# Kernel optimization log

Hardware: AMD Instinct MI355X
Metric: run time of the kernel (lower is better)

The kernel has to match this reference:

```python
import jax, jax.numpy as jnp
import numpy as np

B, N, F_DIM = 64, 4096, 64
K_SLOTS, D, N_ITERS = 8, 64, 3
EPS = 1e-8
LN_EPS = 1e-5  # torch LayerNorm default


def layernorm(x, g, b):
    mu = jnp.mean(x, axis=-1, keepdims=True)
    var = jnp.mean(jnp.square(x - mu), axis=-1, keepdims=True)
    return (x - mu) * jax.lax.rsqrt(var + LN_EPS) * g + b


def gru_cell(x, h, w_ih, w_hh, b_ih, b_hh):
    # torch.nn.GRUCell semantics; weights are [3D, D] with gate order r, z, n
    gi = x @ w_ih.T + b_ih
    gh = h @ w_hh.T + b_hh
    i_r, i_z, i_n = jnp.split(gi, 3, axis=-1)
    h_r, h_z, h_n = jnp.split(gh, 3, axis=-1)
    r = jax.nn.sigmoid(i_r + h_r)
    z = jax.nn.sigmoid(i_z + h_z)
    n = jnp.tanh(i_n + r * h_n)
    return (1.0 - z) * n + z * h


def setup_inputs() -> dict:
    key = jax.random.key(0)
    ks = jax.random.split(key, 16)
    f32 = jnp.float32
    s = 0.05  # small init scale for weights
    return {
        "inputs": jax.random.normal(ks[0], (B, N, F_DIM), f32),
        "slots_noise": jax.random.normal(ks[1], (B, K_SLOTS, D), f32),
        "slots_mu": jax.random.normal(ks[2], (1, 1, D), f32) * s,
        "slots_log_sigma": jax.random.normal(ks[3], (1, 1, D), f32) * s,
        "Wq": jax.random.normal(ks[4], (D, D), f32) * s,
        "Wk": jax.random.normal(ks[5], (D, F_DIM), f32) * s,
        "Wv": jax.random.normal(ks[6], (D, F_DIM), f32) * s,
        "gru_w_ih": jax.random.normal(ks[7], (3 * D, D), f32) * s,
        "gru_w_hh": jax.random.normal(ks[8], (3 * D, D), f32) * s,
        "gru_b_ih": jnp.zeros((3 * D,), f32),
        "gru_b_hh": jnp.zeros((3 * D,), f32),
        "mlp_w1": jax.random.normal(ks[9], (2 * D, D), f32) * s,
        "mlp_b1": jnp.zeros((2 * D,), f32),
        "mlp_w2": jax.random.normal(ks[10], (D, 2 * D), f32) * s,
        "mlp_b2": jnp.zeros((D,), f32),
        "ln_in_g": jnp.ones((F_DIM,), f32), "ln_in_b": jnp.zeros((F_DIM,), f32),
        "ln_slots_g": jnp.ones((D,), f32), "ln_slots_b": jnp.zeros((D,), f32),
        "ln_mlp_g": jnp.ones((D,), f32), "ln_mlp_b": jnp.zeros((D,), f32),
    }


def reference(inputs, slots_noise, slots_mu, slots_log_sigma, Wq, Wk, Wv,
              gru_w_ih, gru_w_hh, gru_b_ih, gru_b_hh,
              mlp_w1, mlp_b1, mlp_w2, mlp_b2,
              ln_in_g, ln_in_b, ln_slots_g, ln_slots_b, ln_mlp_g, ln_mlp_b):
    x = layernorm(inputs, ln_in_g, ln_in_b)          # [B, N, F]
    k = jnp.einsum('bnf,df->bnd', x, Wk)             # [B, N, D]
    v = jnp.einsum('bnf,df->bnd', x, Wv)             # [B, N, D]

    slots = slots_mu + jnp.exp(slots_log_sigma) * slots_noise  # [B, K, D]
    scale = D ** -0.5

    for _ in range(N_ITERS):
        slots_prev = slots
        s_n = layernorm(slots, ln_slots_g, ln_slots_b)
        q = jnp.einsum('bkd,ed->bke', s_n, Wq)                  # [B, K, D]
        attn_logits = jnp.einsum('bnd,bkd->bnk', k, q) * scale  # [B, N, K]
        attn = jax.nn.softmax(attn_logits, axis=-1) + EPS       # softmax over slots
        attn = attn / jnp.sum(attn, axis=1, keepdims=True)      # renormalize over N
        updates = jnp.einsum('bnk,bnd->bkd', attn, v)           # [B, K, D]
        slots = gru_cell(updates.reshape(-1, D), slots_prev.reshape(-1, D),
                         gru_w_ih, gru_w_hh, gru_b_ih, gru_b_hh).reshape(B, K_SLOTS, D)
        h = layernorm(slots, ln_mlp_g, ln_mlp_b)
        h = jax.nn.relu(h @ mlp_w1.T + mlp_b1) @ mlp_w2.T + mlp_b2
        slots = slots + h
    return slots
```

## Files before the change

### kernel.cpp

```cpp
#include <hip/hip_runtime.h>
#include <math.h>

#define NN 4096
#define LN_EPS 1e-5f
#define EPS 1e-8f

typedef unsigned short ushortT;
typedef unsigned int uintT;
typedef __attribute__((ext_vector_type(8))) short short8;
typedef __attribute__((ext_vector_type(4))) float f32x4;
typedef __attribute__((ext_vector_type(4))) unsigned short us4;

#define OFF_KT    0L
#define OFF_V     16777216L
#define OFF_QT    33554432L
#define OFF_ACC   33587200L
#define OFF_COL   33619968L
#define OFF_SLOTS 33620480L
#define OFF_WIHT  33653248L
#define OFF_WHHT  33665536L
#define OFF_W1T   33677824L
#define OFF_W2T   33686016L
#define OFF_WQT   33694208L
#define OFF_WKV   33698304L

__device__ __forceinline__ float wredsum(float v) {
#pragma unroll
  for (int off = 32; off > 0; off >>= 1) v += __shfl_xor(v, off);
  return v;
}

__device__ __forceinline__ ushortT f2bf(float f) {
  uintT b = __float_as_uint(f);
  b += 0x7fff + ((b >> 16) & 1);
  return (ushortT)(b >> 16);
}

__global__ __launch_bounds__(256) void k_prep(
    const float* __restrict__ w_ih, const float* __restrict__ w_hh,
    const float* __restrict__ w1, const float* __restrict__ w2,
    const float* __restrict__ Wq,
    const float* __restrict__ Wk, const float* __restrict__ Wv,
    float* __restrict__ wihT, float* __restrict__ whhT,
    float* __restrict__ w1T, float* __restrict__ w2T, float* __restrict__ wqT,
    ushortT* __restrict__ wpack)
{
  int idx = blockIdx.x * 256 + threadIdx.x;
  if (idx < 12288) {
    int j = idx >> 6, f = idx & 63;
    wihT[f * 192 + j] = w_ih[idx];
  } else if (idx < 24576) {
    int i = idx - 12288; int j = i >> 6, f = i & 63;
    whhT[f * 192 + j] = w_hh[i];
  } else if (idx < 32768) {
    int i = idx - 24576; int j = i >> 6, f = i & 63;
    w1T[f * 128 + j] = w1[i];
  } else if (idx < 40960) {
    int i = idx - 32768; int d = i >> 7, j = i & 127;
    w2T[j * 64 + d] = w2[i];
  } else if (idx < 45056) {
    int i = idx - 40960; int e = i >> 6, d = i & 63;
    wqT[d * 64 + e] = Wq[i];
  } else if (idx < 53248) {
    int i = idx - 45056;
    int j = i & 7, l = (i >> 3) & 63, t2 = i >> 9;
    int ct = t2 >> 1, kb = t2 & 1;
    int kf = kb * 32 + ((l >> 4) << 3) + j;
    int col = (ct << 4) | (l & 15);
    float val = (col < 64) ? Wk[col * 64 + kf] : Wv[(col - 64) * 64 + kf];
    wpack[i] = f2bf(val);
  }
}

__global__ __launch_bounds__(256) void k_ln_project(
    const float* __restrict__ inp, const ushortT* __restrict__ wpack,
    const float* __restrict__ g, const float* __restrict__ bbv,
    ushortT* __restrict__ ktF, ushortT* __restrict__ vF)
{
  __shared__ __align__(16) ushortT xnF[4096];
  __shared__ __align__(16) ushortT kS[4096];
  const int tid = threadIdx.x;
  const int lane = tid & 63;
  const int wave = tid >> 6;
  const int l15 = lane & 15, q = lane >> 4;
  const int tile = blockIdx.x;
  const int b = tile >> 6;
  const int c = tile & 63;
  const int n0 = c << 6;
  const float* rowbase = inp + (((long)b * NN + n0) << 6);
  const float4 g4 = *(const float4*)&g[l15 << 2];
  const float4 b4 = *(const float4*)&bbv[l15 << 2];

#pragma unroll
  for (int i = 0; i < 4; ++i) {
    const int row = (wave << 4) + (i << 2) + q;
    float4 x = *(const float4*)&rowbase[(row << 6) + (l15 << 2)];
    float s = x.x + x.y + x.z + x.w;
    s += __shfl_xor(s, 1); s += __shfl_xor(s, 2);
    s += __shfl_xor(s, 4); s += __shfl_xor(s, 8);
    const float mu = s * (1.f / 64.f);
    float4 dx = {x.x - mu, x.y - mu, x.z - mu, x.w - mu};
    float ss = dx.x * dx.x + dx.y * dx.y + dx.z * dx.z + dx.w * dx.w;
    ss += __shfl_xor(ss, 1); ss += __shfl_xor(ss, 2);
    ss += __shfl_xor(ss, 4); ss += __shfl_xor(ss, 8);
    const float rs = rsqrtf(ss * (1.f / 64.f) + LN_EPS);
    us4 p = {f2bf(dx.x * rs * g4.x + b4.x), f2bf(dx.y * rs * g4.y + b4.y),
             f2bf(dx.z * rs * g4.z + b4.z), f2bf(dx.w * rs * g4.w + b4.w)};
    *(us4*)&xnF[((((wave << 1) + (l15 >> 3)) << 6) + (((l15 & 7) >> 1) << 4)
                 + (row & 15)) * 8 + ((l15 & 1) << 2)] = p;
  }

  short8 bfrag[2][2];
#pragma unroll
  for (int nt = 0; nt < 2; ++nt)
#pragma unroll
    for (int kb = 0; kb < 2; ++kb)
      bfrag[nt][kb] = *(const short8*)&wpack[((((2 * wave + nt) << 1) | kb) * 64 + lane) << 3];

  __syncthreads();

  f32x4 acc[4][2];
#pragma unroll
  for (int mt = 0; mt < 4; ++mt)
#pragma unroll
    for (int nt = 0; nt < 2; ++nt) acc[mt][nt] = (f32x4){0.f, 0.f, 0.f, 0.f};

#pragma unroll
  for (int mt = 0; mt < 4; ++mt) {
    short8 a0 = *(const short8*)&xnF[((mt * 2 + 0) * 64 + lane) << 3];
    short8 a1 = *(const short8*)&xnF[((mt * 2 + 1) * 64 + lane) << 3];
#pragma unroll
    for (int nt = 0; nt < 2; ++nt) {
      acc[mt][nt] = __builtin_amdgcn_mfma_f32_16x16x32_bf16(a0, bfrag[nt][0], acc[mt][nt], 0, 0, 0);
      acc[mt][nt] = __builtin_amdgcn_mfma_f32_16x16x32_bf16(a1, bfrag[nt][1], acc[mt][nt], 0, 0, 0);
    }
  }

  if (wave < 2) {
#pragma unroll
    for (int mt = 0; mt < 4; ++mt)
#pragma unroll
      for (int nt = 0; nt < 2; ++nt) {
        const int base = (((mt * 2 + wave) << 6) + ((2 * nt + (l15 >> 3)) << 4) + (q << 2));
#pragma unroll
        for (int r = 0; r < 4; ++r)
          kS[((base + r) << 3) + (l15 & 7)] = f2bf(acc[mt][nt][r]);
      }
  } else {
    ushortT* vbase = vF + ((long)(b * 64 + c) << 12);
#pragma unroll
    for (int mt = 0; mt < 4; ++mt)
#pragma unroll
      for (int nt = 0; nt < 2; ++nt) {
        const int ntg = 2 * (wave - 2) + nt;
        us4 p = {f2bf(acc[mt][nt][0]), f2bf(acc[mt][nt][1]),
                 f2bf(acc[mt][nt][2]), f2bf(acc[mt][nt][3])};
        *(us4*)&vbase[(((((ntg << 1) + (mt >> 1)) << 6)
                        + (((mt & 1) * 2 + (q >> 1)) << 4) + l15) << 3)
                      + ((q & 1) << 2)] = p;
      }
  }
  __syncthreads();

  ushortT* kdst = ktF + ((long)(b * 64 + c) << 12);
  short8 v0 = *(const short8*)&kS[tid << 4];
  short8 v1 = *(const short8*)&kS[(tid << 4) + 8];
  *(short8*)&kdst[tid << 4] = v0;
  *(short8*)&kdst[(tid << 4) + 8] = v1;
}

__global__ __launch_bounds__(256) void k_init(
    const float* __restrict__ noise, const float* __restrict__ smu,
    const float* __restrict__ slsig, const float* __restrict__ wqT,
    const float* __restrict__ g_sl, const float* __restrict__ b_sl,
    float* __restrict__ slots, ushortT* __restrict__ qF,
    float* __restrict__ acc, float* __restrict__ colsum)
{
  __shared__ float S[4][64];
  const int tid = threadIdx.x, lane = tid & 63, wave = tid >> 6;
  const int row = blockIdx.x * 4 + wave;
  const int b = row >> 3, ks = row & 7;

  float s0 = fmaf(expf(slsig[lane]), noise[row * 64 + lane], smu[lane]);
  slots[row * 64 + lane] = s0;
  acc[row * 64 + lane] = 0.f;
  if (lane == 0) colsum[row] = 0.f;

  float mu = wredsum(s0) * (1.f / 64.f);
  float dx = s0 - mu;
  float var = wredsum(dx * dx) * (1.f / 64.f);
  float sn = dx * rsqrtf(var + LN_EPS) * g_sl[lane] + b_sl[lane];
  S[wave][lane] = sn;
  __syncthreads();
  float qe = 0.f;
#pragma unroll 16
  for (int d = 0; d < 64; ++d) qe = fmaf(S[wave][d], wqT[d * 64 + lane], qe);
  const int kb = lane >> 5, lrow = (lane & 31) >> 3, j = lane & 7;
  qF[((((b * 2 + kb) << 6) + (lrow << 4) + ks) << 3) + j] = f2bf(qe * 0.125f);
  qF[((((b * 2 + kb) << 6) + (lrow << 4) + 8 + ks) << 3) + j] = 0;
}

__global__ __launch_bounds__(256) void k_attn(
    const ushortT* __restrict__ ktF, const ushortT* __restrict__ vF,
    const ushortT* __restrict__ qF,
    float* __restrict__ acc, float* __restrict__ colsum)
{
  __shared__ __align__(16) ushortT attnF[4][1024];
  __shared__ float accLds[4][8][64];
  __shared__ float colLds[4][8];
  const int tid = threadIdx.x;
  const int lane = tid & 63;
  const int wave = tid >> 6;
  const int l15 = lane & 15, q = lane >> 4;
  const int b = blockIdx.x >> 4;
  const int chunk = ((blockIdx.x & 15) << 2) | wave;

  const ushortT* kbF = ktF + ((long)(b * 64 + chunk) << 12);
  const ushortT* vbF = vF + ((long)(b * 64 + chunk) << 12);

  short8 kA[4][2];
#pragma unroll
  for (int mt = 0; mt < 4; ++mt)
#pragma unroll
    for (int kb = 0; kb < 2; ++kb)
      kA[mt][kb] = *(const short8*)&kbF[((mt * 2 + kb) * 64 + lane) << 3];
  short8 qB[2];
#pragma unroll
  for (int kb = 0; kb < 2; ++kb)
    qB[kb] = *(const short8*)&qF[(((b * 2 + kb) << 6) + lane) << 3];

  f32x4 accL[4];
#pragma unroll
  for (int mt = 0; mt < 4; ++mt) {
    accL[mt] = (f32x4){0.f, 0.f, 0.f, 0.f};
    accL[mt] = __builtin_amdgcn_mfma_f32_16x16x32_bf16(kA[mt][0], qB[0], accL[mt], 0, 0, 0);
    accL[mt] = __builtin_amdgcn_mfma_f32_16x16x32_bf16(kA[mt][1], qB[1], accL[mt], 0, 0, 0);
  }

  short8 vB[4][2];
#pragma unroll
  for (int nt = 0; nt < 4; ++nt)
#pragma unroll
    for (int ks = 0; ks < 2; ++ks)
      vB[nt][ks] = *(const short8*)&vbF[((nt * 2 + ks) * 64 + lane) << 3];

  float csum = 0.f;
#pragma unroll
  for (int mt = 0; mt < 4; ++mt) {
    float av[4];
#pragma unroll
    for (int r = 0; r < 4; ++r) {
      float lv = accL[mt][r];
      float mx = lv;
      mx = fmaxf(mx, __shfl_xor(mx, 1));
      mx = fmaxf(mx, __shfl_xor(mx, 2));
      mx = fmaxf(mx, __shfl_xor(mx, 4));
      float ev = __expf(lv - mx);
      float sv = ev;
      sv += __shfl_xor(sv, 1); sv += __shfl_xor(sv, 2); sv += __shfl_xor(sv, 4);
      float a = ev * (1.f / sv) + EPS;
      av[r] = a;
      csum += a;
    }
    us4 p = {f2bf(av[0]), f2bf(av[1]), f2bf(av[2]), f2bf(av[3])};
    *(us4*)&attnF[wave][((((mt >> 1) << 6) + (((mt & 1) * 2 + (q >> 1)) << 4)
                          + l15) << 3) + ((q & 1) << 2)] = p;
  }
  csum += __shfl_xor(csum, 16);
  csum += __shfl_xor(csum, 32);

  short8 pA0 = *(const short8*)&attnF[wave][(0 * 64 + lane) << 3];
  short8 pA1 = *(const short8*)&attnF[wave][(1 * 64 + lane) << 3];

  f32x4 accP[4];
#pragma unroll
  for (int nt = 0; nt < 4; ++nt) {
    accP[nt] = (f32x4){0.f, 0.f, 0.f, 0.f};
    accP[nt] = __builtin_amdgcn_mfma_f32_16x16x32_bf16(pA0, vB[nt][0], accP[nt], 0, 0, 0);
    accP[nt] = __builtin_amdgcn_mfma_f32_16x16x32_bf16(pA1, vB[nt][1], accP[nt], 0, 0, 0);
  }

  if (q < 2) {
#pragma unroll
    for (int nt = 0; nt < 4; ++nt)
#pragma unroll
      for (int r = 0; r < 4; ++r)
        accLds[wave][q * 4 + r][nt * 16 + l15] = accP[nt][r];
  }
  if (q == 0 && l15 < 8) colLds[wave][l15] = csum;
  __syncthreads();

#pragma unroll
  for (int r = 0; r < 2; ++r) {
    const int o = tid + r * 256;
    const int kk = o >> 6, d = o & 63;
    float s = accLds[0][kk][d] + accLds[1][kk][d] + accLds[2][kk][d] + accLds[3][kk][d];
    atomicAdd(&acc[(b * 8 + kk) * 64 + d], s);
  }
  if (tid < 8) {
    float s = colLds[0][tid] + colLds[1][tid] + colLds[2][tid] + colLds[3][tid];
    atomicAdd(&colsum[b * 8 + tid], s);
  }
}

__global__ __launch_bounds__(256) void k_update(
    float* __restrict__ acc, float* __restrict__ colsum,
    float* __restrict__ slots,
    const float* __restrict__ wihT, const float* __restrict__ whhT,
    const float* __restrict__ w1T, const float* __restrict__ w2T,
    const float* __restrict__ wqT,
    const float* __restrict__ b_ih, const float* __restrict__ b_hh,
    const float* __restrict__ mb1, const float* __restrict__ mb2,
    const float* __restrict__ g_ml, const float* __restrict__ b_ml,
    const float* __restrict__ g_sl, const float* __restrict__ b_sl,
    ushortT* __restrict__ qF, float* __restrict__ dout)
{
  __shared__ float S[4][256];
  const int tid = threadIdx.x, lane = tid & 63, wave = tid >> 6;
  const int row = blockIdx.x * 4 + wave;
  const int b = row >> 3, ks = row & 7;

  const float csum = colsum[row];
  const float u = acc[row * 64 + lane] / csum;
  const float h = slots[row * 64 + lane];
  acc[row * 64 + lane] = 0.f;
  if (lane == 0) colsum[row] = 0.f;

  float* Su = &S[wave][0];
  float* Sh = &S[wave][64];
  Su[lane] = u; Sh[lane] = h;
  __syncthreads();

  float gir = b_ih[lane], giz = b_ih[64 + lane], gin = b_ih[128 + lane];
  float ghr = b_hh[lane], ghz = b_hh[64 + lane], ghn = b_hh[128 + lane];
#pragma unroll 4
  for (int f = 0; f < 64; ++f) {
    const float uf = Su[f], hf = Sh[f];
    gir = fmaf(uf, wihT[f * 192 + lane], gir);
    giz = fmaf(uf, wihT[f * 192 + 64 + lane], giz);
    gin = fmaf(uf, wihT[f * 192 + 128 + lane], gin);
    ghr = fmaf(hf, whhT[f * 192 + lane], ghr);
    ghz = fmaf(hf, whhT[f * 192 + 64 + lane], ghz);
    ghn = fmaf(hf, whhT[f * 192 + 128 + lane], ghn);
  }
  const float r = 1.f / (1.f + expf(-(gir + ghr)));
  const float z = 1.f / (1.f + expf(-(giz + ghz)));
  const float nn = tanhf(fmaf(r, ghn, gin));
  const float hnew = (1.f - z) * nn + z * h;

  float mu = wredsum(hnew) * (1.f / 64.f);
  float dx = hnew - mu;
  float var = wredsum(dx * dx) * (1.f / 64.f);
  const float ln = dx * rsqrtf(var + LN_EPS) * g_ml[lane] + b_ml[lane];
  float* Sln = &S[wave][128];
  Sln[lane] = ln;
  __syncthreads();

  float h1a = mb1[lane], h1b = mb1[64 + lane];
#pragma unroll 4
  for (int f = 0; f < 64; ++f) {
    const float lf = Sln[f];
    h1a = fmaf(lf, w1T[f * 128 + lane], h1a);
    h1b = fmaf(lf, w1T[f * 128 + 64 + lane], h1b);
  }
  h1a = fmaxf(h1a, 0.f); h1b = fmaxf(h1b, 0.f);
  __syncthreads();
  float* Shid = &S[wave][0];
  Shid[lane] = h1a; Shid[64 + lane] = h1b;
  __syncthreads();

  float o = mb2[lane];
#pragma unroll 4
  for (int j = 0; j < 128; ++j) o = fmaf(Shid[j], w2T[j * 64 + lane], o);
  const float snew = hnew + o;
  slots[row * 64 + lane] = snew;
  if (dout) dout[row * 64 + lane] = snew;

  float mu2 = wredsum(snew) * (1.f / 64.f);
  float dx2 = snew - mu2;
  float v2 = wredsum(dx2 * dx2) * (1.f / 64.f);
  const float sq = dx2 * rsqrtf(v2 + LN_EPS) * g_sl[lane] + b_sl[lane];
  __syncthreads();
  float* Ssq = &S[wave][128];
  Ssq[lane] = sq;
  __syncthreads();
  float qe = 0.f;
#pragma unroll 16
  for (int d = 0; d < 64; ++d) qe = fmaf(Ssq[d], wqT[d * 64 + lane], qe);
  const int kb = lane >> 5, lrow = (lane & 31) >> 3, j = lane & 7;
  qF[((((b * 2 + kb) << 6) + (lrow << 4) + ks) << 3) + j] = f2bf(qe * 0.125f);
}

extern "C" void kernel_launch(void* const* d_in, const int* in_sizes, int n_in,
                              void* d_out, int out_size, void* d_ws, size_t ws_size,
                              hipStream_t stream) {
  const float* inp   = (const float*)d_in[0];
  const float* noise = (const float*)d_in[1];
  const float* smu   = (const float*)d_in[2];
  const float* slsig = (const float*)d_in[3];
  const float* Wq    = (const float*)d_in[4];
  const float* Wk    = (const float*)d_in[5];
  const float* Wv    = (const float*)d_in[6];
  const float* w_ih  = (const float*)d_in[7];
  const float* w_hh  = (const float*)d_in[8];
  const float* b_ih  = (const float*)d_in[9];
  const float* b_hh  = (const float*)d_in[10];
  const float* w1    = (const float*)d_in[11];
  const float* b1    = (const float*)d_in[12];
  const float* w2    = (const float*)d_in[13];
  const float* b2    = (const float*)d_in[14];
  const float* g_in  = (const float*)d_in[15];
  const float* bi_in = (const float*)d_in[16];
  const float* g_sl  = (const float*)d_in[17];
  const float* bi_sl = (const float*)d_in[18];
  const float* g_ml  = (const float*)d_in[19];
  const float* bi_ml = (const float*)d_in[20];

  float* ws      = (float*)d_ws;
  ushortT* ktF   = (ushortT*)(ws + OFF_KT);
  ushortT* vF    = (ushortT*)(ws + OFF_V);
  ushortT* qF    = (ushortT*)(ws + OFF_QT);
  float* ac      = ws + OFF_ACC;
  float* cs      = ws + OFF_COL;
  float* sl      = ws + OFF_SLOTS;
  float* wihT    = ws + OFF_WIHT;
  float* whhT    = ws + OFF_WHHT;
  float* w1T     = ws + OFF_W1T;
  float* w2T     = ws + OFF_W2T;
  float* wqT     = ws + OFF_WQT;
  ushortT* wpk   = (ushortT*)(ws + OFF_WKV);

  k_prep<<<208, 256, 0, stream>>>(w_ih, w_hh, w1, w2, Wq, Wk, Wv,
                                  wihT, whhT, w1T, w2T, wqT, wpk);
  k_ln_project<<<4096, 256, 0, stream>>>(inp, wpk, g_in, bi_in, ktF, vF);
  k_init<<<128, 256, 0, stream>>>(noise, smu, slsig, wqT, g_sl, bi_sl, sl, qF, ac, cs);
  for (int it = 0; it < 3; ++it) {
    k_attn<<<1024, 256, 0, stream>>>(ktF, vF, qF, ac, cs);
    k_update<<<128, 256, 0, stream>>>(ac, cs, sl, wihT, whhT, w1T, w2T, wqT,
                                      b_ih, b_hh, b1, b2, g_ml, bi_ml, g_sl, bi_sl,
                                      qF, it == 2 ? (float*)d_out : nullptr);
  }
}
```

Baseline: 243.3 us.

## Fuse slot update into attention via last-block counter and merge init into LN kernel

Removes the separate k_update launch by having the last of the 16 attention blocks per batch, detected with an atomic counter, perform the GRU, MLP and next-query computation, two slots per wave. It also folds the slot initialisation into the LN/projection kernel as extra blocks, which cuts two launches per iteration structure down to one. The cost is a tail of serial update work on a single block per batch, plus threadfence and atomic overhead. The counter must be reset correctly for the next iteration.

```diff
diff --git a/kernel.cpp b/kernel.cpp
--- a/kernel.cpp
+++ b/kernel.cpp
@@ -23,6 +23,7 @@
 #define OFF_W2T   33686016L
 #define OFF_WQT   33694208L
 #define OFF_WKV   33698304L
+#define OFF_CNT   33702400L
 
 __device__ __forceinline__ float wredsum(float v) {
 #pragma unroll
@@ -43,7 +44,7 @@
     const float* __restrict__ Wk, const float* __restrict__ Wv,
     float* __restrict__ wihT, float* __restrict__ whhT,
     float* __restrict__ w1T, float* __restrict__ w2T, float* __restrict__ wqT,
-    ushortT* __restrict__ wpack)
+    ushortT* __restrict__ wpack, uintT* __restrict__ cnt)
 {
   int idx = blockIdx.x * 256 + threadIdx.x;
   if (idx < 12288) {
@@ -69,19 +70,53 @@
     int col = (ct << 4) | (l & 15);
     float val = (col < 64) ? Wk[col * 64 + kf] : Wv[(col - 64) * 64 + kf];
     wpack[i] = f2bf(val);
-  }
-}
-
-__global__ __launch_bounds__(256) void k_ln_project(
+  } else if (idx < 53312) {
+    cnt[idx - 53248] = 0u;
+  }
+}
+
+__global__ __launch_bounds__(256) void k_ln_init(
     const float* __restrict__ inp, const ushortT* __restrict__ wpack,
     const float* __restrict__ g, const float* __restrict__ bbv,
-    ushortT* __restrict__ ktF, ushortT* __restrict__ vF)
+    ushortT* __restrict__ ktF, ushortT* __restrict__ vF,
+    const float* __restrict__ noise, const float* __restrict__ smu,
+    const float* __restrict__ slsig, const float* __restrict__ wqT,
+    const float* __restrict__ g_sl, const float* __restrict__ b_sl,
+    float* __restrict__ slots, ushortT* __restrict__ qF,
+    float* __restrict__ acc, float* __restrict__ colsum)
 {
   __shared__ __align__(16) ushortT xnF[4096];
   __shared__ __align__(16) ushortT kS[4096];
   const int tid = threadIdx.x;
   const int lane = tid & 63;
   const int wave = tid >> 6;
+
+  if (blockIdx.x >= 4096) {
+    const int bi = blockIdx.x - 4096;
+    const int row = bi * 4 + wave;
+    const int b = row >> 3, ks = row & 7;
+    float* S2 = (float*)&xnF[0];
+
+    float s0 = fmaf(expf(slsig[lane]), noise[row * 64 + lane], smu[lane]);
+    slots[row * 64 + lane] = s0;
+    acc[row * 64 + lane] = 0.f;
+    if (lane == 0) colsum[row] = 0.f;
+
+    float mu = wredsum(s0) * (1.f / 64.f);
+    float dx = s0 - mu;
+    float var = wredsum(dx * dx) * (1.f / 64.f);
+    float sn = dx * rsqrtf(var + LN_EPS) * g_sl[lane] + b_sl[lane];
+    S2[(wave << 6) + lane] = sn;
+    __syncthreads();
+    float qe = 0.f;
+#pragma unroll 16
+    for (int d = 0; d < 64; ++d) qe = fmaf(S2[(wave << 6) + d], wqT[d * 64 + lane], qe);
+    const int kb = lane >> 5, lrow = (lane & 31) >> 3, j = lane & 7;
+    qF[((((b * 2 + kb) << 6) + (lrow << 4) + ks) << 3) + j] = f2bf(qe * 0.125f);
+    qF[((((b * 2 + kb) << 6) + (lrow << 4) + 8 + ks) << 3) + j] = 0;
+    return;
+  }
+
   const int l15 = lane & 15, q = lane >> 4;
   const int tile = blockIdx.x;
   const int b = tile >> 6;
@@ -119,11 +154,11 @@
 
   __syncthreads();
 
-  f32x4 acc[4][2];
+  f32x4 acc4[4][2];
 #pragma unroll
   for (int mt = 0; mt < 4; ++mt)
 #pragma unroll
-    for (int nt = 0; nt < 2; ++nt) acc[mt][nt] = (f32x4){0.f, 0.f, 0.f, 0.f};
+    for (int nt = 0; nt < 2; ++nt) acc4[mt][nt] = (f32x4){0.f, 0.f, 0.f, 0.f};
 
 #pragma unroll
   for (int mt = 0; mt < 4; ++mt) {
@@ -131,8 +166,8 @@
     short8 a1 = *(const short8*)&xnF[((mt * 2 + 1) * 64 + lane) << 3];
 #pragma unroll
     for (int nt = 0; nt < 2; ++nt) {
-      acc[mt][nt] = __builtin_amdgcn_mfma_f32_16x16x32_bf16(a0, bfrag[nt][0], acc[mt][nt], 0, 0, 0);
-      acc[mt][nt] = __builtin_amdgcn_mfma_f32_16x16x32_bf16(a1, bfrag[nt][1], acc[mt][nt], 0, 0, 0);
+      acc4[mt][nt] = __builtin_amdgcn_mfma_f32_16x16x32_bf16(a0, bfrag[nt][0], acc4[mt][nt], 0, 0, 0);
+      acc4[mt][nt] = __builtin_amdgcn_mfma_f32_16x16x32_bf16(a1, bfrag[nt][1], acc4[mt][nt], 0, 0, 0);
     }
   }
 
@@ -144,7 +179,7 @@
         const int base = (((mt * 2 + wave) << 6) + ((2 * nt + (l15 >> 3)) << 4) + (q << 2));
 #pragma unroll
         for (int r = 0; r < 4; ++r)
-          kS[((base + r) << 3) + (l15 & 7)] = f2bf(acc[mt][nt][r]);
+          kS[((base + r) << 3) + (l15 & 7)] = f2bf(acc4[mt][nt][r]);
       }
   } else {
     ushortT* vbase = vF + ((long)(b * 64 + c) << 12);
@@ -153,8 +188,8 @@
 #pragma unroll
       for (int nt = 0; nt < 2; ++nt) {
         const int ntg = 2 * (wave - 2) + nt;
-        us4 p = {f2bf(acc[mt][nt][0]), f2bf(acc[mt][nt][1]),
-                 f2bf(acc[mt][nt][2]), f2bf(acc[mt][nt][3])};
+        us4 p = {f2bf(acc4[mt][nt][0]), f2bf(acc4[mt][nt][1]),
+                 f2bf(acc4[mt][nt][2]), f2bf(acc4[mt][nt][3])};
         *(us4*)&vbase[(((((ntg << 1) + (mt >> 1)) << 6)
                         + (((mt & 1) * 2 + (q >> 1)) << 4) + l15) << 3)
                       + ((q & 1) << 2)] = p;
@@ -169,45 +204,24 @@
   *(short8*)&kdst[(tid << 4) + 8] = v1;
 }
 
-__global__ __launch_bounds__(256) void k_init(
-    const float* __restrict__ noise, const float* __restrict__ smu,
-    const float* __restrict__ slsig, const float* __restrict__ wqT,
-    const float* __restrict__ g_sl, const float* __restrict__ b_sl,
-    float* __restrict__ slots, ushortT* __restrict__ qF,
-    float* __restrict__ acc, float* __restrict__ colsum)
-{
-  __shared__ float S[4][64];
-  const int tid = threadIdx.x, lane = tid & 63, wave = tid >> 6;
-  const int row = blockIdx.x * 4 + wave;
-  const int b = row >> 3, ks = row & 7;
-
-  float s0 = fmaf(expf(slsig[lane]), noise[row * 64 + lane], smu[lane]);
-  slots[row * 64 + lane] = s0;
-  acc[row * 64 + lane] = 0.f;
-  if (lane == 0) colsum[row] = 0.f;
-
-  float mu = wredsum(s0) * (1.f / 64.f);
-  float dx = s0 - mu;
-  float var = wredsum(dx * dx) * (1.f / 64.f);
-  float sn = dx * rsqrtf(var + LN_EPS) * g_sl[lane] + b_sl[lane];
-  S[wave][lane] = sn;
-  __syncthreads();
-  float qe = 0.f;
-#pragma unroll 16
-  for (int d = 0; d < 64; ++d) qe = fmaf(S[wave][d], wqT[d * 64 + lane], qe);
-  const int kb = lane >> 5, lrow = (lane & 31) >> 3, j = lane & 7;
-  qF[((((b * 2 + kb) << 6) + (lrow << 4) + ks) << 3) + j] = f2bf(qe * 0.125f);
-  qF[((((b * 2 + kb) << 6) + (lrow << 4) + 8 + ks) << 3) + j] = 0;
-}
-
 __global__ __launch_bounds__(256) void k_attn(
     const ushortT* __restrict__ ktF, const ushortT* __restrict__ vF,
-    const ushortT* __restrict__ qF,
-    float* __restrict__ acc, float* __restrict__ colsum)
+    ushortT* __restrict__ qF,
+    float* __restrict__ acc, float* __restrict__ colsum,
+    uintT* __restrict__ cnt, float* __restrict__ slots,
+    const float* __restrict__ wihT, const float* __restrict__ whhT,
+    const float* __restrict__ w1T, const float* __restrict__ w2T,
+    const float* __restrict__ wqT,
+    const float* __restrict__ b_ih, const float* __restrict__ b_hh,
+    const float* __restrict__ mb1, const float* __restrict__ mb2,
+    const float* __restrict__ g_ml, const float* __restrict__ b_ml,
+    const float* __restrict__ g_sl, const float* __restrict__ b_sl,
+    float* __restrict__ dout)
 {
   __shared__ __align__(16) ushortT attnF[4][1024];
   __shared__ float accLds[4][8][64];
   __shared__ float colLds[4][8];
+  __shared__ int lastFlag;
   const int tid = threadIdx.x;
   const int lane = tid & 63;
   const int wave = tid >> 6;
@@ -301,94 +315,121 @@
     float s = colLds[0][tid] + colLds[1][tid] + colLds[2][tid] + colLds[3][tid];
     atomicAdd(&colsum[b * 8 + tid], s);
   }
-}
-
-__global__ __launch_bounds__(256) void k_update(
-    float* __restrict__ acc, float* __restrict__ colsum,
-    float* __restrict__ slots,
-    const float* __restrict__ wihT, const float* __restrict__ whhT,
-    const float* __restrict__ w1T, const float* __restrict__ w2T,
-    const float* __restrict__ wqT,
-    const float* __restrict__ b_ih, const float* __restrict__ b_hh,
-    const float* __restrict__ mb1, const float* __restrict__ mb2,
-    const float* __restrict__ g_ml, const float* __restrict__ b_ml,
-    const float* __restrict__ g_sl, const float* __restrict__ b_sl,
-    ushortT* __restrict__ qF, float* __restrict__ dout)
-{
-  __shared__ float S[4][256];
-  const int tid = threadIdx.x, lane = tid & 63, wave = tid >> 6;
-  const int row = blockIdx.x * 4 + wave;
-  const int b = row >> 3, ks = row & 7;
-
-  const float csum = colsum[row];
-  const float u = acc[row * 64 + lane] / csum;
-  const float h = slots[row * 64 + lane];
-  acc[row * 64 + lane] = 0.f;
-  if (lane == 0) colsum[row] = 0.f;
-
-  float* Su = &S[wave][0];
-  float* Sh = &S[wave][64];
-  Su[lane] = u; Sh[lane] = h;
+
+  __threadfence();
   __syncthreads();
-
-  float gir = b_ih[lane], giz = b_ih[64 + lane], gin = b_ih[128 + lane];
-  float ghr = b_hh[lane], ghz = b_hh[64 + lane], ghn = b_hh[128 + lane];
+  if (tid == 0) lastFlag = (atomicAdd(&cnt[b], 1u) == 15u);
+  __syncthreads();
+  if (!lastFlag) return;
+
+  const int ks0 = wave, ks1 = wave + 4;
+  const int row0 = b * 8 + ks0, row1 = b * 8 + ks1;
+
+  float csv0 = 0.f, csv1 = 0.f;
+  if (lane == 0) {
+    csv0 = atomicAdd(&colsum[row0], 0.f);
+    csv1 = atomicAdd(&colsum[row1], 0.f);
+  }
+  csv0 = __shfl(csv0, 0); csv1 = __shfl(csv1, 0);
+  const float u0 = atomicAdd(&acc[row0 * 64 + lane], 0.f) / csv0;
+  const float u1 = atomicAdd(&acc[row1 * 64 + lane], 0.f) / csv1;
+  const float h0 = slots[row0 * 64 + lane];
+  const float h1 = slots[row1 * 64 + lane];
+
+  float* S = (float*)&attnF[wave][0];
+  S[lane] = u0; S[64 + lane] = u1; S[128 + lane] = h0; S[192 + lane] = h1;
+
+  float gir0 = b_ih[lane], giz0 = b_ih[64 + lane], gin0 = b_ih[128 + lane];
+  float ghr0 = b_hh[lane], ghz0 = b_hh[64 + lane], ghn0 = b_hh[128 + lane];
+  float gir1 = gir0, giz1 = giz0, gin1 = gin0;
+  float ghr1 = ghr0, ghz1 = ghz0, ghn1 = ghn0;
 #pragma unroll 4
   for (int f = 0; f < 64; ++f) {
-    const float uf = Su[f], hf = Sh[f];
-    gir = fmaf(uf, wihT[f * 192 + lane], gir);
-    giz = fmaf(uf, wihT[f * 192 + 64 + lane], giz);
-    gin = fmaf(uf, wihT[f * 192 + 128 + lane], gin);
-    ghr = fmaf(hf, whhT[f * 192 + lane], ghr);
-    ghz = fmaf(hf, whhT[f * 192 + 64 + lane], ghz);
-    ghn = fmaf(hf, whhT[f * 192 + 128 + lane], ghn);
-  }
-  const float r = 1.f / (1.f + expf(-(gir + ghr)));
-  const float z = 1.f / (1.f + expf(-(giz + ghz)));
-  const float nn = tanhf(fmaf(r, ghn, gin));
-  const float hnew = (1.f - z) * nn + z * h;
-
-  float mu = wredsum(hnew) * (1.f / 64.f);
-  float dx = hnew - mu;
-  float var = wredsum(dx * dx) * (1.f / 64.f);
-  const float ln = dx * rsqrtf(var + LN_EPS) * g_ml[lane] + b_ml[lane];
-  float* Sln = &S[wave][128];
-  Sln[lane] = ln;
-  __syncthreads();
-
-  float h1a = mb1[lane], h1b = mb1[64 + lane];
+    const float wr = wihT[f * 192 + lane], wz = wihT[f * 192 + 64 + lane],
+                wn = wihT[f * 192 + 128 + lane];
+    const float vr = whhT[f * 192 + lane], vz = whhT[f * 192 + 64 + lane],
+                vn = whhT[f * 192 + 128 + lane];
+    const float a0 = S[f], a1 = S[64 + f], c0 = S[128 + f], c1 = S[192 + f];
+    gir0 = fmaf(a0, wr, gir0); gir1 = fmaf(a1, wr, gir1);
+    giz0 = fmaf(a0, wz, giz0); giz1 = fmaf(a1, wz, giz1);
+    gin0 = fmaf(a0, wn, gin0); gin1 = fmaf(a1, wn, gin1);
+    ghr0 = fmaf(c0, vr, ghr0); ghr1 = fmaf(c1, vr, ghr1);
+    ghz0 = fmaf(c0, vz, ghz0); ghz1 = fmaf(c1, vz, ghz1);
+    ghn0 = fmaf(c0, vn, ghn0); ghn1 = fmaf(c1, vn, ghn1);
+  }
+  const float r0 = 1.f / (1.f + expf(-(gir0 + ghr0)));
+  const float z0 = 1.f / (1.f + expf(-(giz0 + ghz0)));
+  const float n0 = tanhf(fmaf(r0, ghn0, gin0));
+  const float hn0 = (1.f - z0) * n0 + z0 * h0;
+  const float r1 = 1.f / (1.f + expf(-(gir1 + ghr1)));
+  const float z1 = 1.f / (1.f + expf(-(giz1 + ghz1)));
+  const float n1 = tanhf(fmaf(r1, ghn1, gin1));
+  const float hn1 = (1.f - z1) * n1 + z1 * h1;
+
+  float mu0 = wredsum(hn0) * (1.f / 64.f);
+  float dx0 = hn0 - mu0;
+  float va0 = wredsum(dx0 * dx0) * (1.f / 64.f);
+  const float ln0 = dx0 * rsqrtf(va0 + LN_EPS) * g_ml[lane] + b_ml[lane];
+  float mu1 = wredsum(hn1) * (1.f / 64.f);
+  float dx1 = hn1 - mu1;
+  float va1 = wredsum(dx1 * dx1) * (1.f / 64.f);
+  const float ln1 = dx1 * rsqrtf(va1 + LN_EPS) * g_ml[lane] + b_ml[lane];
+  S[256 + lane] = ln0; S[320 + lane] = ln1;
+
+  float h1a0 = mb1[lane], h1b0 = mb1[64 + lane];
+  float h1a1 = h1a0, h1b1 = h1b0;
 #pragma unroll 4
   for (int f = 0; f < 64; ++f) {
-    const float lf = Sln[f];
-    h1a = fmaf(lf, w1T[f * 128 + lane], h1a);
-    h1b = fmaf(lf, w1T[f * 128 + 64 + lane], h1b);
-  }
-  h1a = fmaxf(h1a, 0.f); h1b = fmaxf(h1b, 0.f);
-  __syncthreads();
-  float* Shid = &S[wave][0];
-  Shid[lane] = h1a; Shid[64 + lane] = h1b;
-  __syncthreads();
-
-  float o = mb2[lane];
+    const float wa = w1T[f * 128 + lane], wb = w1T[f * 128 + 64 + lane];
+    const float l0 = S[256 + f], l1 = S[320 + f];
+    h1a0 = fmaf(l0, wa, h1a0); h1a1 = fmaf(l1, wa, h1a1);
+    h1b0 = fmaf(l0, wb, h1b0); h1b1 = fmaf(l1, wb, h1b1);
+  }
+  h1a0 = fmaxf(h1a0, 0.f); h1b0 = fmaxf(h1b0, 0.f);
+  h1a1 = fmaxf(h1a1, 0.f); h1b1 = fmaxf(h1b1, 0.f);
+  S[lane] = h1a0; S[64 + lane] = h1b0;
+  S[128 + lane] = h1a1; S[192 + lane] = h1b1;
+
+  float o0 = mb2[lane], o1 = mb2[lane];
 #pragma unroll 4
-  for (int j = 0; j < 128; ++j) o = fmaf(Shid[j], w2T[j * 64 + lane], o);
-  const float snew = hnew + o;
-  slots[row * 64 + lane] = snew;
-  if (dout) dout[row * 64 + lane] = snew;
-
-  float mu2 = wredsum(snew) * (1.f / 64.f);
-  float dx2 = snew - mu2;
-  float v2 = wredsum(dx2 * dx2) * (1.f / 64.f);
-  const float sq = dx2 * rsqrtf(v2 + LN_EPS) * g_sl[lane] + b_sl[lane];
-  __syncthreads();
-  float* Ssq = &S[wave][128];
-  Ssq[lane] = sq;
-  __syncthreads();
-  float qe = 0.f;
-#pragma unroll 16
-  for (int d = 0; d < 64; ++d) qe = fmaf(Ssq[d], wqT[d * 64 + lane], qe);
-  const int kb = lane >> 5, lrow = (lane & 31) >> 3, j = lane & 7;
-  qF[((((b * 2 + kb) << 6) + (lrow << 4) + ks) << 3) + j] = f2bf(qe * 0.125f);
+  for (int j = 0; j < 128; ++j) {
+    const float w2v = w2T[j * 64 + lane];
+    o0 = fmaf(S[j], w2v, o0);
+    o1 = fmaf(S[128 + j], w2v, o1);
+  }
+  const float sn0 = hn0 + o0;
+  const float sn1 = hn1 + o1;
+  slots[row0 * 64 + lane] = sn0;
+  slots[row1 * 64 + lane] = sn1;
+  if (dout) {
+    dout[row0 * 64 + lane] = sn0;
+    dout[row1 * 64 + lane] = sn1;
+  }
+
+  float m20 = wredsum(sn0) * (1.f / 64.f);
+  float d20 = sn0 - m20;
+  float v20 = wredsum(d20 * d20) * (1.f / 64.f);
+  const float sq0 = d20 * rsqrtf(v20 + LN_EPS) * g_sl[lane] + b_sl[lane];
+  float m21 = wredsum(sn1) * (1.f / 64.f);
+  float d21 = sn1 - m21;
+  float v21 = wredsum(d21 * d21) * (1.f / 64.f);
+  const float sq1 = d21 * rsqrtf(v21 + LN_EPS) * g_sl[lane] + b_sl[lane];
+  S[256 + lane] = sq0; S[320 + lane] = sq1;
+  float qe0 = 0.f, qe1 = 0.f;
+#pragma unroll 8
+  for (int d = 0; d < 64; ++d) {
+    const float wq = wqT[d * 64 + lane];
+    qe0 = fmaf(S[256 + d], wq, qe0);
+    qe1 = fmaf(S[320 + d], wq, qe1);
+  }
+  const int kb = lane >> 5, lrow = (lane & 31) >> 3, jj = lane & 7;
+  qF[((((b * 2 + kb) << 6) + (lrow << 4) + ks0) << 3) + jj] = f2bf(qe0 * 0.125f);
+  qF[((((b * 2 + kb) << 6) + (lrow << 4) + ks1) << 3) + jj] = f2bf(qe1 * 0.125f);
+
+  acc[row0 * 64 + lane] = 0.f;
+  acc[row1 * 64 + lane] = 0.f;
+  if (lane == 0) { colsum[row0] = 0.f; colsum[row1] = 0.f; }
+  if (tid == 0) cnt[b] = 0u;
 }
 
 extern "C" void kernel_launch(void* const* d_in, const int* in_sizes, int n_in,
@@ -429,15 +470,17 @@
   float* w2T     = ws + OFF_W2T;
   float* wqT     = ws + OFF_WQT;
   ushortT* wpk   = (ushortT*)(ws + OFF_WKV);
-
-  k_prep<<<208, 256, 0, stream>>>(w_ih, w_hh, w1, w2, Wq, Wk, Wv,
-                                  wihT, whhT, w1T, w2T, wqT, wpk);
-  k_ln_project<<<4096, 256, 0, stream>>>(inp, wpk, g_in, bi_in, ktF, vF);
-  k_init<<<128, 256, 0, stream>>>(noise, smu, slsig, wqT, g_sl, bi_sl, sl, qF, ac, cs);
+  uintT* cnt     = (uintT*)(ws + OFF_CNT);
+
+  k_prep<<<209, 256, 0, stream>>>(w_ih, w_hh, w1, w2, Wq, Wk, Wv,
+                                  wihT, whhT, w1T, w2T, wqT, wpk, cnt);
+  k_ln_init<<<4224, 256, 0, stream>>>(inp, wpk, g_in, bi_in, ktF, vF,
+                                      noise, smu, slsig, wqT, g_sl, bi_sl,
+                                      sl, qF, ac, cs);
   for (int it = 0; it < 3; ++it) {
-    k_attn<<<1024, 256, 0, stream>>>(ktF, vF, qF, ac, cs);
-    k_update<<<128, 256, 0, stream>>>(ac, cs, sl, wihT, whhT, w1T, w2T, wqT,
-                                      b_ih, b_hh, b1, b2, g_ml, bi_ml, g_sl, bi_sl,
-                                      qF, it == 2 ? (float*)d_out : nullptr);
-  }
-}
+    k_attn<<<1024, 256, 0, stream>>>(ktF, vF, qF, ac, cs, cnt, sl,
+                                     wihT, whhT, w1T, w2T, wqT,
+                                     b_ih, b_hh, b1, b2, g_ml, bi_ml, g_sl, bi_sl,
+                                     it == 2 ? (float*)d_out : nullptr);
+  }
+}
```

Measured after the change: 528.6 us. +117.3%, slower.
